# Kernel tuning notes

Hardware: AMD Instinct MI355X
Metric: run time of the kernel (lower is better)

Reference implementation:

```python
import jax, jax.numpy as jnp
import numpy as np

HEADS = 16
EPS = 1e-5

def _ln(x, g, b):
    m = jnp.mean(x, axis=-1, keepdims=True)
    v = jnp.mean((x - m) ** 2, axis=-1, keepdims=True)
    return (x - m) * jax.lax.rsqrt(v + EPS) * g + b

def setup_inputs() -> dict:
    key = jax.random.key(0)
    ks = jax.random.split(key, 12)
    B, N, C, H = 4, 2048, 1024, 4096
    d = {}
    d['x'] = jax.random.normal(ks[0], (B, N, C), jnp.float32)
    d['pos_embed'] = jax.random.normal(ks[1], (1, N, C), jnp.float32)
    # LayerNorm params (normq, normk, normv, norm)
    for nm in ['nq', 'nk', 'nv', 'n']:
        d[nm + '_g'] = jnp.ones((C,), jnp.float32)
        d[nm + '_b'] = jnp.zeros((C,), jnp.float32)
    s = 1.0 / np.sqrt(C)
    d['wq'] = jax.random.uniform(ks[2], (C, C), jnp.float32, -s, s)
    d['bq'] = jnp.zeros((C,), jnp.float32)
    d['wk'] = jax.random.uniform(ks[3], (C, C), jnp.float32, -s, s)
    d['bk'] = jnp.zeros((C,), jnp.float32)
    d['wv'] = jax.random.uniform(ks[4], (C, C), jnp.float32, -s, s)
    d['bv'] = jnp.zeros((C,), jnp.float32)
    d['wp'] = jax.random.uniform(ks[5], (C, C), jnp.float32, -s, s)
    d['bp'] = jnp.zeros((C,), jnp.float32)
    d['w1'] = jax.random.uniform(ks[6], (C, H), jnp.float32, -s, s)
    d['b1'] = jnp.zeros((H,), jnp.float32)
    sh = 1.0 / np.sqrt(H)
    d['w2'] = jax.random.uniform(ks[7], (H, C), jnp.float32, -sh, sh)
    d['b2'] = jnp.zeros((C,), jnp.float32)
    return d

def reference(x, pos_embed, nq_g, nq_b, nk_g, nk_b, nv_g, nv_b, wq, bq, wk, bk, wv, bv, wp, bp, n_g, n_b, w1, b1, w2, b2):
    B, N, C = x.shape
    hd = C // HEADS
    scale = hd ** -0.5
    q_in = x
    k_in = x + pos_embed
    v_in = x + pos_embed
    # Attention (eval mode: dropout = identity)
    q = (_ln(q_in, nq_g, nq_b) @ wq + bq).reshape(B, N, HEADS, hd)
    k = (_ln(k_in, nk_g, nk_b) @ wk + bk).reshape(B, N, HEADS, hd)
    v = (_ln(v_in, nv_g, nv_b) @ wv + bv).reshape(B, N, HEADS, hd)
    attn = jnp.einsum('bqhd,bkhd->bhqk', q, k) * scale
    attn = jax.nn.softmax(attn, axis=-1)
    out = jnp.einsum('bhqk,bkhd->bqhd', attn, v).reshape(B, N, C)
    out = out @ wp + bp
    # residual + MLP
    h = q_in + out
    y = _ln(h, n_g, n_b) @ w1 + b1
    y = jnp.where(y >= 0, y, 0.1 * y)  # LeakyReLU(0.1)
    y = y @ w2 + b2
    return h + y
```

## Files before the change

### kernel.cpp

```cpp
#include <hip/hip_runtime.h>
#include <hip/hip_bf16.h>

#define DEV __device__ __forceinline__

typedef __attribute__((ext_vector_type(8))) short short8;
typedef __attribute__((ext_vector_type(4))) short short4v;
typedef __attribute__((ext_vector_type(4))) float f32x4;
typedef __attribute__((ext_vector_type(2))) int int2v;

constexpr int Bb   = 4;
constexpr int SEQ  = 2048;
constexpr int C    = 1024;
constexpr int HID  = 4096;
constexpr int NH   = 16;
constexpr int HD   = 64;
constexpr int MTOT = Bb * SEQ;

DEV unsigned bfbits(float f) {
  unsigned x = __float_as_uint(f);
  return (x + 0x7fffu + ((x >> 16) & 1u)) >> 16;
}

DEV short f2bf(float f) { return (short)bfbits(f); }

DEV unsigned packrn(float a, float b) {
  unsigned ua = __float_as_uint(a) + 0x8000u;
  unsigned ub = __float_as_uint(b) + 0x8000u;
  return __builtin_amdgcn_perm(ub, ua, 0x07060302u);
}

DEV float fexp2(float x) {
#if __has_builtin(__builtin_amdgcn_exp2f)
  return __builtin_amdgcn_exp2f(x);
#else
  float r;
  asm("v_exp_f32 %0, %1" : "=v"(r) : "v"(x));
  return r;
#endif
}

DEV void gload16(const void* g, void* l) {
  __builtin_amdgcn_global_load_lds((const __attribute__((address_space(1))) void*)g,
                                   (__attribute__((address_space(3))) void*)l, 16, 0, 0);
}

DEV f32x4 mfma16(short4v a, short4v b, f32x4 c) {
#if __has_builtin(__builtin_amdgcn_mfma_f32_16x16x16bf16_1k)
  return __builtin_amdgcn_mfma_f32_16x16x16bf16_1k(a, b, c, 0, 0, 0);
#else
  asm volatile("v_mfma_f32_16x16x16_bf16 %0, %1, %2, %0" : "+v"(c) : "v"(a), "v"(b));
  return c;
#endif
}

DEV void transpose_body(const float* __restrict__ src, short* __restrict__ dst,
                        int R, int Cc) {
  __shared__ float t[32][33];
  int tx = threadIdx.x & 31, ty = threadIdx.x >> 5;
  int c0 = blockIdx.x * 32, r0 = blockIdx.y * 32;
  #pragma unroll
  for (int i = 0; i < 4; i++)
    t[ty + i * 8][tx] = src[(size_t)(r0 + ty + i * 8) * Cc + c0 + tx];
  __syncthreads();
  #pragma unroll
  for (int i = 0; i < 4; i++)
    dst[(size_t)(c0 + ty + i * 8) * R + r0 + tx] = f2bf(t[tx][ty + i * 8]);
}

__global__ void k_transpose_w(const float* __restrict__ src, short* __restrict__ dst,
                              int R, int Cc) {
  transpose_body(src, dst, R, Cc);
}

__global__ void k_transpose_w4(const float* __restrict__ s0, const float* __restrict__ s1,
                               const float* __restrict__ s2, const float* __restrict__ s3,
                               short* __restrict__ d0, short* __restrict__ d1,
                               short* __restrict__ d2, short* __restrict__ d3) {
  const float* s = blockIdx.z == 0 ? s0 : blockIdx.z == 1 ? s1 : blockIdx.z == 2 ? s2 : s3;
  short*       d = blockIdx.z == 0 ? d0 : blockIdx.z == 1 ? d1 : blockIdx.z == 2 ? d2 : d3;
  transpose_body(s, d, C, C);
}

__global__ void k_transpose_v(const short* __restrict__ V, short* __restrict__ Vt) {
  __shared__ short t[32][33];
  int tx = threadIdx.x & 31, ty = threadIdx.x >> 5;
  int plane = blockIdx.z;
  int b = plane >> 4, h = plane & 15;
  int n0 = blockIdx.x * 32, d0 = blockIdx.y * 32;
  #pragma unroll
  for (int i = 0; i < 4; i++)
    t[ty + i * 8][tx] = V[(size_t)(b * SEQ + n0 + ty + i * 8) * C + h * HD + d0 + tx];
  __syncthreads();
  #pragma unroll
  for (int i = 0; i < 4; i++)
    Vt[((size_t)plane * HD + d0 + ty + i * 8) * SEQ + n0 + tx] = t[tx][ty + i * 8];
}

__global__ void k_ln_qkv(const float* __restrict__ x, const float* __restrict__ pos,
                         const float* __restrict__ nqg, const float* __restrict__ nqb,
                         const float* __restrict__ nkg, const float* __restrict__ nkb,
                         const float* __restrict__ nvg, const float* __restrict__ nvb,
                         short* __restrict__ xq, short* __restrict__ xk,
                         short* __restrict__ xv) {
  int row = blockIdx.x, tid = threadIdx.x;
  int n = row & (SEQ - 1);
  float a4[4], p4[4];
  float s1 = 0, s2 = 0, t1 = 0, t2 = 0;
  #pragma unroll
  for (int i = 0; i < 4; i++) {
    int c = tid + i * 256;
    float a = x[(size_t)row * C + c];
    float p = pos[(size_t)n * C + c] + a;
    a4[i] = a; p4[i] = p;
    s1 += a; s2 += a * a; t1 += p; t2 += p * p;
  }
  #pragma unroll
  for (int off = 32; off; off >>= 1) {
    s1 += __shfl_xor(s1, off, 64);
    s2 += __shfl_xor(s2, off, 64);
    t1 += __shfl_xor(t1, off, 64);
    t2 += __shfl_xor(t2, off, 64);
  }
  __shared__ float red[4][4];
  int wave = tid >> 6, lane = tid & 63;
  if (lane == 0) { red[wave][0] = s1; red[wave][1] = s2; red[wave][2] = t1; red[wave][3] = t2; }
  __syncthreads();
  s1 = red[0][0] + red[1][0] + red[2][0] + red[3][0];
  s2 = red[0][1] + red[1][1] + red[2][1] + red[3][1];
  t1 = red[0][2] + red[1][2] + red[2][2] + red[3][2];
  t2 = red[0][3] + red[1][3] + red[2][3] + red[3][3];
  float mq = s1 * (1.f / C), mk = t1 * (1.f / C);
  float rq = rsqrtf(s2 * (1.f / C) - mq * mq + 1e-5f);
  float rk = rsqrtf(t2 * (1.f / C) - mk * mk + 1e-5f);
  #pragma unroll
  for (int i = 0; i < 4; i++) {
    int c = tid + i * 256;
    float nq_ = (a4[i] - mq) * rq;
    float nk_ = (p4[i] - mk) * rk;
    xq[(size_t)row * C + c] = f2bf(nq_ * nqg[c] + nqb[c]);
    xk[(size_t)row * C + c] = f2bf(nk_ * nkg[c] + nkb[c]);
    xv[(size_t)row * C + c] = f2bf(nk_ * nvg[c] + nvb[c]);
  }
}

__global__ void k_ln1(const float* __restrict__ h, const float* __restrict__ g,
                      const float* __restrict__ bta, short* __restrict__ out) {
  int row = blockIdx.x, tid = threadIdx.x;
  float a4[4];
  float s1 = 0, s2 = 0;
  #pragma unroll
  for (int i = 0; i < 4; i++) {
    int c = tid + i * 256;
    float a = h[(size_t)row * C + c];
    a4[i] = a; s1 += a; s2 += a * a;
  }
  #pragma unroll
  for (int off = 32; off; off >>= 1) {
    s1 += __shfl_xor(s1, off, 64);
    s2 += __shfl_xor(s2, off, 64);
  }
  __shared__ float red[4][2];
  int wave = tid >> 6, lane = tid & 63;
  if (lane == 0) { red[wave][0] = s1; red[wave][1] = s2; }
  __syncthreads();
  s1 = red[0][0] + red[1][0] + red[2][0] + red[3][0];
  s2 = red[0][1] + red[1][1] + red[2][1] + red[3][1];
  float m = s1 * (1.f / C);
  float r = rsqrtf(s2 * (1.f / C) - m * m + 1e-5f);
  #pragma unroll
  for (int i = 0; i < 4; i++) {
    int c = tid + i * 256;
    out[(size_t)row * C + c] = f2bf((a4[i] - m) * r * g[c] + bta[c]);
  }
}

template <typename EPI>
DEV void gemm_body(const short* __restrict__ A, const short* __restrict__ Bt,
                   int Kk, short* sA, short* sB, EPI&& epi) {
  const int tid = threadIdx.x;
  const int wave = tid >> 6, lane = tid & 63, quad = lane >> 4, l15 = lane & 15;
  const int wm = (wave >> 1) * 64, wn = (wave & 1) * 64;
  constexpr int BO = 128 * 32;

  const int r0 = tid >> 2, s0 = (tid & 3) * 8;
  const short* gA0 = A + (size_t)r0 * Kk + s0;
  const short* gA1 = A + (size_t)(r0 + 64) * Kk + s0;
  const short* gB0 = Bt + (size_t)r0 * Kk + s0;
  const short* gB1 = Bt + (size_t)(r0 + 64) * Kk + s0;
  short* lA0 = &sA[tid * 8];
  short* lA1 = &sA[(tid + 256) * 8];
  short* lB0 = &sB[tid * 8];
  short* lB1 = &sB[(tid + 256) * 8];

  const f32x4 fzero = {0.f, 0.f, 0.f, 0.f};
  f32x4 acc[4][4];
  #pragma unroll
  for (int mi = 0; mi < 4; mi++)
    #pragma unroll
    for (int ni = 0; ni < 4; ni++) acc[mi][ni] = fzero;

  gload16(gA0, lA0);
  gload16(gA1, lA1);
  gload16(gB0, lB0);
  gload16(gB1, lB1);

  for (int k0 = 0; k0 < Kk; k0 += 32) {
    const int buf = (k0 >> 5) & 1;
    __syncthreads();
    if (k0 + 32 < Kk) {
      const int bo = (buf ^ 1) * BO;
      gload16(gA0 + k0 + 32, lA0 + bo);
      gload16(gA1 + k0 + 32, lA1 + bo);
      gload16(gB0 + k0 + 32, lB0 + bo);
      gload16(gB1 + k0 + 32, lB1 + bo);
    }
    const int bo = buf * BO;
    short8 av[4], bv[4];
    #pragma unroll
    for (int mi = 0; mi < 4; mi++)
      av[mi] = *(const short8*)&sA[bo + (wm + mi * 16 + l15) * 32 + quad * 8];
    #pragma unroll
    for (int ni = 0; ni < 4; ni++)
      bv[ni] = *(const short8*)&sB[bo + (wn + ni * 16 + l15) * 32 + quad * 8];
    #pragma unroll
    for (int mi = 0; mi < 4; mi++)
      #pragma unroll
      for (int ni = 0; ni < 4; ni++)
        acc[mi][ni] = __builtin_amdgcn_mfma_f32_16x16x32_bf16(av[mi], bv[ni], acc[mi][ni], 0, 0, 0);
  }
  epi(acc, wm, wn, quad, l15);
}

template <int MODE>
__global__ __launch_bounds__(256, 2)
void k_gemm(const short* __restrict__ A, const short* __restrict__ Bt,
            const float* __restrict__ bias, const float* __restrict__ resid,
            void* __restrict__ outp, int Nn, int Kk) {
  __shared__ short sA[2 * 128 * 32];
  __shared__ short sB[2 * 128 * 32];
  const int m0 = blockIdx.x * 128, n0 = blockIdx.y * 128;
  gemm_body(A + (size_t)m0 * Kk, Bt + (size_t)n0 * Kk, Kk, sA, sB,
    [&](f32x4 (&acc)[4][4], int wm, int wn, int quad, int l15) {
      float bb[4];
      #pragma unroll
      for (int ni = 0; ni < 4; ni++) bb[ni] = bias[n0 + wn + ni * 16 + l15];
      #pragma unroll
      for (int mi = 0; mi < 4; mi++) {
        #pragma unroll
        for (int ni = 0; ni < 4; ni++) {
          #pragma unroll
          for (int r = 0; r < 4; r++) {
            int row = m0 + wm + mi * 16 + quad * 4 + r;
            int col = n0 + wn + ni * 16 + l15;
            float v = acc[mi][ni][r] + bb[ni];
            if constexpr (MODE == 1) v = v >= 0.f ? v : 0.1f * v;
            if constexpr (MODE == 2)
              ((float*)outp)[(size_t)row * Nn + col] = resid[(size_t)row * Nn + col] + v;
            else
              ((short*)outp)[(size_t)row * Nn + col] = f2bf(v);
          }
        }
      }
    });
}

template <int MODE>
__global__ __launch_bounds__(256, 2)
void k_gemm_p3(const short* __restrict__ A, const short* __restrict__ Bt,
               const float* __restrict__ bias, const float* __restrict__ resid,
               void* __restrict__ outp, int Nn, int Kk) {
  __shared__ short sA[3 * 128 * 32];
  __shared__ short sB[3 * 128 * 32];
  constexpr int BO = 128 * 32;
  const int tid = threadIdx.x;
  const int wave = tid >> 6, lane = tid & 63, quad = lane >> 4, l15 = lane & 15;
  const int wm = (wave >> 1) * 64, wn = (wave & 1) * 64;
  const int m0 = blockIdx.x * 128, n0 = blockIdx.y * 128;
  const short* Ab = A + (size_t)m0 * Kk;
  const short* Bb_ = Bt + (size_t)n0 * Kk;

  const int r0 = tid >> 2, s0 = (tid & 3) * 8;
  const short* gA0 = Ab + (size_t)r0 * Kk + s0;
  const short* gA1 = Ab + (size_t)(r0 + 64) * Kk + s0;
  const short* gB0 = Bb_ + (size_t)r0 * Kk + s0;
  const short* gB1 = Bb_ + (size_t)(r0 + 64) * Kk + s0;
  short* lA0 = &sA[tid * 8];
  short* lA1 = &sA[(tid + 256) * 8];
  short* lB0 = &sB[tid * 8];
  short* lB1 = &sB[(tid + 256) * 8];

  const f32x4 fzero = {0.f, 0.f, 0.f, 0.f};
  f32x4 acc[4][4];
  #pragma unroll
  for (int mi = 0; mi < 4; mi++)
    #pragma unroll
    for (int ni = 0; ni < 4; ni++) acc[mi][ni] = fzero;

  const int nk = Kk >> 5;

#define STG(j) {                                        \
    const int bo_ = ((j) % 3) * BO;                     \
    const int kk_ = (j) << 5;                           \
    gload16(gA0 + kk_, lA0 + bo_);                      \
    gload16(gA1 + kk_, lA1 + bo_);                      \
    gload16(gB0 + kk_, lB0 + bo_);                      \
    gload16(gB1 + kk_, lB1 + bo_); }

  STG(0)
  if (nk > 1) STG(1)

  for (int k = 0; k < nk; k++) {
    if (k + 1 < nk) asm volatile("s_waitcnt vmcnt(4)" ::: "memory");
    else            asm volatile("s_waitcnt vmcnt(0)" ::: "memory");
    __builtin_amdgcn_s_barrier();
    if (k + 2 < nk) STG(k + 2)
    const int bo = (k % 3) * BO;
    short8 av[4], bv[4];
    #pragma unroll
    for (int mi = 0; mi < 4; mi++)
      av[mi] = *(const short8*)&sA[bo + (wm + mi * 16 + l15) * 32 + quad * 8];
    #pragma unroll
    for (int ni = 0; ni < 4; ni++)
      bv[ni] = *(const short8*)&sB[bo + (wn + ni * 16 + l15) * 32 + quad * 8];
    #pragma unroll
    for (int mi = 0; mi < 4; mi++)
      #pragma unroll
      for (int ni = 0; ni < 4; ni++)
        acc[mi][ni] = __builtin_amdgcn_mfma_f32_16x16x32_bf16(av[mi], bv[ni], acc[mi][ni], 0, 0, 0);
  }
#undef STG

  float bb[4];
  #pragma unroll
  for (int ni = 0; ni < 4; ni++) bb[ni] = bias[n0 + wn + ni * 16 + l15];
  #pragma unroll
  for (int mi = 0; mi < 4; mi++) {
    #pragma unroll
    for (int ni = 0; ni < 4; ni++) {
      #pragma unroll
      for (int r = 0; r < 4; r++) {
        int row = m0 + wm + mi * 16 + quad * 4 + r;
        int col = n0 + wn + ni * 16 + l15;
        float v = acc[mi][ni][r] + bb[ni];
        if constexpr (MODE == 1) v = v >= 0.f ? v : 0.1f * v;
        if constexpr (MODE == 2)
          ((float*)outp)[(size_t)row * Nn + col] = resid[(size_t)row * Nn + col] + v;
        else
          ((short*)outp)[(size_t)row * Nn + col] = f2bf(v);
      }
    }
  }
}

__global__ __launch_bounds__(256, 2)
void k_gemm_qkv(const short* __restrict__ xq, const short* __restrict__ xk,
                const short* __restrict__ xv,
                const short* __restrict__ wqT, const short* __restrict__ wkT,
                const short* __restrict__ wvT,
                const float* __restrict__ bq, const float* __restrict__ bk,
                const float* __restrict__ bv,
                short* __restrict__ Qm, short* __restrict__ Km, short* __restrict__ Vm) {
  __shared__ short sA[2 * 128 * 32];
  __shared__ short sB[2 * 128 * 32];
  const int z = blockIdx.z;
  const short* A    = z == 0 ? xq : z == 1 ? xk : xv;
  const short* Bt   = z == 0 ? wqT : z == 1 ? wkT : wvT;
  const float* bias = z == 0 ? bq : z == 1 ? bk : bv;
  short* outp       = z == 0 ? Qm : z == 1 ? Km : Vm;
  const float scale = z == 0 ? 0.1803368801111244f : 1.0f;
  const int m0 = blockIdx.x * 128, n0 = blockIdx.y * 128;
  gemm_body(A + (size_t)m0 * C, Bt + (size_t)n0 * C, C, sA, sB,
    [&](f32x4 (&acc)[4][4], int wm, int wn, int quad, int l15) {
      float bb[4];
      #pragma unroll
      for (int ni = 0; ni < 4; ni++) bb[ni] = bias[n0 + wn + ni * 16 + l15];
      #pragma unroll
      for (int mi = 0; mi < 4; mi++)
        #pragma unroll
        for (int ni = 0; ni < 4; ni++)
          #pragma unroll
          for (int r = 0; r < 4; r++) {
            int row = m0 + wm + mi * 16 + quad * 4 + r;
            int col = n0 + wn + ni * 16 + l15;
            outp[(size_t)row * C + col] = f2bf((acc[mi][ni][r] + bb[ni]) * scale);
          }
    });
}

__global__ __launch_bounds__(256, 4)
void k_attn(const short* __restrict__ Q, const short* __restrict__ K,
            const short* __restrict__ Vt, short* __restrict__ O) {
  __shared__ __align__(16) short sK[2][64 * 64];
  __shared__ __align__(16) short sV[2][64 * 64];
  const int tid = threadIdx.x;
  const int bh = blockIdx.x;
  const int b = bh >> 4, h = bh & 15;
  const int q0 = blockIdx.y * 128;
  const int wave = tid >> 6, lane = tid & 63, quad = lane >> 4, l15 = lane & 15;
  const int wm = wave * 32;
  const size_t tokBase = (size_t)b * SEQ;

  short8 qf[2][2];
  #pragma unroll
  for (int qi = 0; qi < 2; qi++)
    #pragma unroll
    for (int hf = 0; hf < 2; hf++)
      qf[qi][hf] = *(const short8*)(Q + (tokBase + q0 + wm + qi * 16 + l15) * C
                                    + h * HD + hf * 32 + quad * 8);

  const int r0 = tid >> 3,        c0s = ((tid & 7) ^ (r0 & 7)) * 8;
  const int r1 = (tid + 256) >> 3, c1s = ((tid & 7) ^ (r1 & 7)) * 8;
  const short* gK0 = K + (tokBase + r0) * C + h * HD + c0s;
  const short* gK1 = K + (tokBase + r1) * C + h * HD + c1s;
  const short* gV0 = Vt + ((size_t)bh * HD + r0) * SEQ + c0s;
  const short* gV1 = Vt + ((size_t)bh * HD + r1) * SEQ + c1s;
  short* lK0 = &sK[0][tid * 8];
  short* lK1 = &sK[0][(tid + 256) * 8];
  short* lV0 = &sV[0][tid * 8];
  short* lV1 = &sV[0][(tid + 256) * 8];
  constexpr int BUFO = 64 * 64;

#define STAGE(bufsel, kb) {                                   \
    int kk = (kb) * 64, bo = (bufsel) * BUFO;                 \
    gload16(gK0 + (size_t)kk * C, lK0 + bo);                  \
    gload16(gK1 + (size_t)kk * C, lK1 + bo);                  \
    gload16(gV0 + kk,             lV0 + bo);                  \
    gload16(gV1 + kk,             lV1 + bo); }

  const f32x4 fzero = {0.f, 0.f, 0.f, 0.f};
  const short4v onesv = {0x3F80, 0x3F80, 0x3F80, 0x3F80};
  f32x4 o[2][4];
  f32x4 oSum[2] = {fzero, fzero};
  #pragma unroll
  for (int qi = 0; qi < 2; qi++)
    #pragma unroll
    for (int di = 0; di < 4; di++) o[qi][di] = fzero;

  const int sw = l15 & 7;

  STAGE(0, 0)

  for (int kb = 0; kb < SEQ / 64; kb++) {
    const int buf = kb & 1;
    __syncthreads();
    if (kb + 1 < SEQ / 64) STAGE(buf ^ 1, kb + 1)

    unsigned pk[4][2][2];
    #pragma unroll
    for (int ki = 0; ki < 4; ki++) {
      const int krow = (ki * 16 + l15) * 64;
      short8 a0 = *(const short8*)&sK[buf][krow + ((0 + quad) ^ sw) * 8];
      short8 a1 = *(const short8*)&sK[buf][krow + ((4 + quad) ^ sw) * 8];
      #pragma unroll
      for (int qi = 0; qi < 2; qi++) {
        f32x4 st = __builtin_amdgcn_mfma_f32_16x16x32_bf16(a0, qf[qi][0], fzero, 0, 0, 0);
        st = __builtin_amdgcn_mfma_f32_16x16x32_bf16(a1, qf[qi][1], st, 0, 0, 0);
        float p0 = fexp2(st[0]), p1 = fexp2(st[1]);
        float p2 = fexp2(st[2]), p3 = fexp2(st[3]);
        pk[ki][qi][0] = packrn(p0, p1);
        pk[ki][qi][1] = packrn(p2, p3);
      }
    }

    #pragma unroll
    for (int ki = 0; ki < 4; ki++) {
      short4v bv[4];
      const int g = ((ki * 2 + (quad >> 1)) ^ sw) * 8 + (quad & 1) * 4;
      #pragma unroll
      for (int di = 0; di < 4; di++)
        bv[di] = *(const short4v*)&sV[buf][(di * 16 + l15) * 64 + g];
      #pragma unroll
      for (int qi = 0; qi < 2; qi++) {
        int2v t; t.x = (int)pk[ki][qi][0]; t.y = (int)pk[ki][qi][1];
        short4v aP = __builtin_bit_cast(short4v, t);
        oSum[qi] = mfma16(aP, onesv, oSum[qi]);
        #pragma unroll
        for (int di = 0; di < 4; di++)
          o[qi][di] = mfma16(aP, bv[di], o[qi][di]);
      }
    }
  }
#undef STAGE

  float linv[2][4];
  #pragma unroll
  for (int qi = 0; qi < 2; qi++)
    #pragma unroll
    for (int r = 0; r < 4; r++)
      linv[qi][r] = 1.0f / oSum[qi][r];

  #pragma unroll
  for (int qi = 0; qi < 2; qi++)
    #pragma unroll
    for (int di = 0; di < 4; di++)
      #pragma unroll
      for (int r = 0; r < 4; r++) {
        int row = q0 + wm + qi * 16 + quad * 4 + r;
        int col = h * HD + di * 16 + l15;
        O[(tokBase + row) * C + col] = f2bf(o[qi][di][r] * linv[qi][r]);
      }
}

extern "C" void kernel_launch(void* const* d_in, const int* in_sizes, int n_in,
                              void* d_out, int out_size, void* d_ws, size_t ws_size,
                              hipStream_t stream) {
  const float* x   = (const float*)d_in[0];
  const float* pos = (const float*)d_in[1];
  const float* nqg = (const float*)d_in[2];
  const float* nqb = (const float*)d_in[3];
  const float* nkg = (const float*)d_in[4];
  const float* nkb = (const float*)d_in[5];
  const float* nvg = (const float*)d_in[6];
  const float* nvb = (const float*)d_in[7];
  const float* ng  = (const float*)d_in[8];
  const float* nb  = (const float*)d_in[9];
  const float* wq  = (const float*)d_in[10];
  const float* bq  = (const float*)d_in[11];
  const float* wk  = (const float*)d_in[12];
  const float* bk  = (const float*)d_in[13];
  const float* wv  = (const float*)d_in[14];
  const float* bv  = (const float*)d_in[15];
  const float* wp  = (const float*)d_in[16];
  const float* bp  = (const float*)d_in[17];
  const float* w1  = (const float*)d_in[18];
  const float* b1  = (const float*)d_in[19];
  const float* w2  = (const float*)d_in[20];
  const float* b2  = (const float*)d_in[21];

  char* ws = (char*)d_ws;
  const size_t MB = 1u << 20;
  short* wqT  = (short*)(ws + 0 * MB);
  short* wkT  = (short*)(ws + 2 * MB);
  short* wvT  = (short*)(ws + 4 * MB);
  short* wpT  = (short*)(ws + 6 * MB);
  short* w1T  = (short*)(ws + 8 * MB);
  short* w2T  = (short*)(ws + 16 * MB);
  short* xq   = (short*)(ws + 24 * MB);
  short* xk   = (short*)(ws + 40 * MB);
  short* xv   = (short*)(ws + 56 * MB);
  short* Qm   = (short*)(ws + 72 * MB);
  short* Km   = (short*)(ws + 88 * MB);
  short* Vm   = (short*)(ws + 104 * MB);
  short* Vt   = (short*)(ws + 120 * MB);
  short* y1   = (short*)(ws + 72 * MB);
  short* Ob   = xk;
  short* hln  = xq;
  float* hbuf = (float*)(ws + 136 * MB);
  (void)ws_size; (void)in_sizes; (void)n_in; (void)out_size;

  dim3 blk(256);
  k_transpose_w4<<<dim3(32, 32, 4), blk, 0, stream>>>(wq, wk, wv, wp, wqT, wkT, wvT, wpT);
  k_transpose_w<<<dim3(128, 32), blk, 0, stream>>>(w1, w1T, C, HID);
  k_transpose_w<<<dim3(32, 128), blk, 0, stream>>>(w2, w2T, HID, C);
  k_ln_qkv<<<dim3(MTOT), blk, 0, stream>>>(x, pos, nqg, nqb, nkg, nkb, nvg, nvb, xq, xk, xv);
  k_gemm_qkv<<<dim3(MTOT / 128, C / 128, 3), blk, 0, stream>>>(xq, xk, xv, wqT, wkT, wvT,
                                                               bq, bk, bv, Qm, Km, Vm);
  k_transpose_v<<<dim3(SEQ / 32, HD / 32, Bb * NH), blk, 0, stream>>>(Vm, Vt);
  k_attn<<<dim3(Bb * NH, SEQ / 128), blk, 0, stream>>>(Qm, Km, Vt, Ob);
  k_gemm<2><<<dim3(MTOT / 128, C / 128), blk, 0, stream>>>(Ob, wpT, bp, x, hbuf, C, C);
  k_ln1<<<dim3(MTOT), blk, 0, stream>>>(hbuf, ng, nb, hln);
  k_gemm<1><<<dim3(MTOT / 128, HID / 128), blk, 0, stream>>>(hln, w1T, b1, nullptr, y1, HID, C);
  k_gemm_p3<2><<<dim3(MTOT / 128, C / 128), blk, 0, stream>>>(y1, w2T, b2, hbuf, (float*)d_out, C, HID);
}
```

Measured before the change: 538.0 us.

## Replace down-projection GEMM with 8-wave 128x256 tile, swizzled LDS and phased MFMA

The final MLP down-projection GEMM (K=4096) moves to a new kernel with 512 threads, a 128x256 output tile, K-step 64, and double buffering. LDS rows are XOR-swizzled to avoid bank conflicts. The MFMA work is split into four barrier-separated phases with raised wave priority, and the block index is remapped for L2 locality. The goal is higher arithmetic intensity and better overlap of loads with MFMAs. In exchange, occupancy drops to one block per CU and the extra per-phase barriers may stall waves.

```diff
diff --git a/kernel.cpp b/kernel.cpp
--- a/kernel.cpp
+++ b/kernel.cpp
@@ -264,30 +264,78 @@
     });
 }
 
+template <int Q>
+DEV void phase8(const short* __restrict__ sAb, const short* __restrict__ sBb,
+                f32x4 (&acc)[4][4], int wm, int wn, int quad, int l15) {
+  constexpr int mis = (Q & 1) * 2, nis = (Q >> 1) * 2;
+  short8 av[2][2], bv[2][2];
+  #pragma unroll
+  for (int m2 = 0; m2 < 2; m2++) {
+    const int rA = wm + (mis + m2) * 16 + l15;
+    const int sw = rA & 7;
+    #pragma unroll
+    for (int ks = 0; ks < 2; ks++)
+      av[m2][ks] = *(const short8*)&sAb[rA * 64 + ((ks * 4 + quad) ^ sw) * 8];
+  }
+  #pragma unroll
+  for (int n2 = 0; n2 < 2; n2++) {
+    const int rB = wn + (nis + n2) * 16 + l15;
+    const int sw = rB & 7;
+    #pragma unroll
+    for (int ks = 0; ks < 2; ks++)
+      bv[n2][ks] = *(const short8*)&sBb[rB * 64 + ((ks * 4 + quad) ^ sw) * 8];
+  }
+  __builtin_amdgcn_s_barrier();
+  asm volatile("s_waitcnt lgkmcnt(0)" ::: "memory");
+  __builtin_amdgcn_sched_barrier(0);
+  __builtin_amdgcn_s_setprio(1);
+  #pragma unroll
+  for (int ks = 0; ks < 2; ks++)
+    #pragma unroll
+    for (int m2 = 0; m2 < 2; m2++)
+      #pragma unroll
+      for (int n2 = 0; n2 < 2; n2++)
+        acc[mis + m2][nis + n2] = __builtin_amdgcn_mfma_f32_16x16x32_bf16(
+            av[m2][ks], bv[n2][ks], acc[mis + m2][nis + n2], 0, 0, 0);
+  __builtin_amdgcn_s_setprio(0);
+  __builtin_amdgcn_s_barrier();
+}
+
 template <int MODE>
-__global__ __launch_bounds__(256, 2)
-void k_gemm_p3(const short* __restrict__ A, const short* __restrict__ Bt,
-               const float* __restrict__ bias, const float* __restrict__ resid,
-               void* __restrict__ outp, int Nn, int Kk) {
-  __shared__ short sA[3 * 128 * 32];
-  __shared__ short sB[3 * 128 * 32];
-  constexpr int BO = 128 * 32;
+__global__ __launch_bounds__(512, 1)
+void k_gemm8(const short* __restrict__ A, const short* __restrict__ Bt,
+             const float* __restrict__ bias, const float* __restrict__ resid,
+             void* __restrict__ outp, int Nn, int Kk) {
+  __shared__ __align__(16) short sA[2][128 * 64];
+  __shared__ __align__(16) short sB[2][256 * 64];
   const int tid = threadIdx.x;
   const int wave = tid >> 6, lane = tid & 63, quad = lane >> 4, l15 = lane & 15;
-  const int wm = (wave >> 1) * 64, wn = (wave & 1) * 64;
-  const int m0 = blockIdx.x * 128, n0 = blockIdx.y * 128;
-  const short* Ab = A + (size_t)m0 * Kk;
-  const short* Bb_ = Bt + (size_t)n0 * Kk;
-
-  const int r0 = tid >> 2, s0 = (tid & 3) * 8;
-  const short* gA0 = Ab + (size_t)r0 * Kk + s0;
-  const short* gA1 = Ab + (size_t)(r0 + 64) * Kk + s0;
-  const short* gB0 = Bb_ + (size_t)r0 * Kk + s0;
-  const short* gB1 = Bb_ + (size_t)(r0 + 64) * Kk + s0;
-  short* lA0 = &sA[tid * 8];
-  short* lA1 = &sA[(tid + 256) * 8];
-  short* lB0 = &sB[tid * 8];
-  short* lB1 = &sB[(tid + 256) * 8];
+  const int wm = (wave >> 2) * 64, wn = (wave & 3) * 64;
+
+  const int gx = gridDim.x;
+  const int nwg = gx * gridDim.y;
+  const int orig = blockIdx.y * gx + blockIdx.x;
+  const int swz = (orig & 7) * (nwg >> 3) + (orig >> 3);
+  const int m0 = (swz % gx) * 128, n0 = (swz / gx) * 256;
+
+  const int sr = tid >> 3, su = tid & 7;
+  const int sx = (su ^ (sr & 7)) * 8;
+  const short* gA0 = A + (size_t)(m0 + sr) * Kk + sx;
+  const short* gA1 = gA0 + (size_t)64 * Kk;
+  const short* gB0 = Bt + (size_t)(n0 + sr) * Kk + sx;
+  const short* gB1 = gB0 + (size_t)64 * Kk;
+  const short* gB2 = gB0 + (size_t)128 * Kk;
+  const short* gB3 = gB0 + (size_t)192 * Kk;
+
+  auto stg = [&](int t) {
+    const int b_ = t & 1, ko = t << 6;
+    gload16(gA0 + ko, &sA[b_][(size_t)tid * 8]);
+    gload16(gA1 + ko, &sA[b_][(size_t)(512 + tid) * 8]);
+    gload16(gB0 + ko, &sB[b_][(size_t)tid * 8]);
+    gload16(gB1 + ko, &sB[b_][(size_t)(512 + tid) * 8]);
+    gload16(gB2 + ko, &sB[b_][(size_t)(1024 + tid) * 8]);
+    gload16(gB3 + ko, &sB[b_][(size_t)(1536 + tid) * 8]);
+  };
 
   const f32x4 fzero = {0.f, 0.f, 0.f, 0.f};
   f32x4 acc[4][4];
@@ -296,39 +344,31 @@
     #pragma unroll
     for (int ni = 0; ni < 4; ni++) acc[mi][ni] = fzero;
 
-  const int nk = Kk >> 5;
-
-#define STG(j) {                                        \
-    const int bo_ = ((j) % 3) * BO;                     \
-    const int kk_ = (j) << 5;                           \
-    gload16(gA0 + kk_, lA0 + bo_);                      \
-    gload16(gA1 + kk_, lA1 + bo_);                      \
-    gload16(gB0 + kk_, lB0 + bo_);                      \
-    gload16(gB1 + kk_, lB1 + bo_); }
-
-  STG(0)
-  if (nk > 1) STG(1)
-
-  for (int k = 0; k < nk; k++) {
-    if (k + 1 < nk) asm volatile("s_waitcnt vmcnt(4)" ::: "memory");
-    else            asm volatile("s_waitcnt vmcnt(0)" ::: "memory");
+  const int nkt = Kk >> 6;
+  stg(0);
+  for (int t = 0; t < nkt; t += 2) {
+    if (t + 1 < nkt) { stg(t + 1); asm volatile("s_waitcnt vmcnt(6)" ::: "memory"); }
+    else             {             asm volatile("s_waitcnt vmcnt(0)" ::: "memory"); }
     __builtin_amdgcn_s_barrier();
-    if (k + 2 < nk) STG(k + 2)
-    const int bo = (k % 3) * BO;
-    short8 av[4], bv[4];
-    #pragma unroll
-    for (int mi = 0; mi < 4; mi++)
-      av[mi] = *(const short8*)&sA[bo + (wm + mi * 16 + l15) * 32 + quad * 8];
-    #pragma unroll
-    for (int ni = 0; ni < 4; ni++)
-      bv[ni] = *(const short8*)&sB[bo + (wn + ni * 16 + l15) * 32 + quad * 8];
-    #pragma unroll
-    for (int mi = 0; mi < 4; mi++)
-      #pragma unroll
-      for (int ni = 0; ni < 4; ni++)
-        acc[mi][ni] = __builtin_amdgcn_mfma_f32_16x16x32_bf16(av[mi], bv[ni], acc[mi][ni], 0, 0, 0);
-  }
-#undef STG
+    {
+      const short* a_ = &sA[t & 1][0]; const short* b_ = &sB[t & 1][0];
+      phase8<0>(a_, b_, acc, wm, wn, quad, l15);
+      phase8<1>(a_, b_, acc, wm, wn, quad, l15);
+      phase8<2>(a_, b_, acc, wm, wn, quad, l15);
+      phase8<3>(a_, b_, acc, wm, wn, quad, l15);
+    }
+    if (t + 1 >= nkt) break;
+    if (t + 2 < nkt) { stg(t + 2); asm volatile("s_waitcnt vmcnt(6)" ::: "memory"); }
+    else             {             asm volatile("s_waitcnt vmcnt(0)" ::: "memory"); }
+    __builtin_amdgcn_s_barrier();
+    {
+      const short* a_ = &sA[(t + 1) & 1][0]; const short* b_ = &sB[(t + 1) & 1][0];
+      phase8<0>(a_, b_, acc, wm, wn, quad, l15);
+      phase8<1>(a_, b_, acc, wm, wn, quad, l15);
+      phase8<2>(a_, b_, acc, wm, wn, quad, l15);
+      phase8<3>(a_, b_, acc, wm, wn, quad, l15);
+    }
+  }
 
   float bb[4];
   #pragma unroll
@@ -560,5 +600,6 @@
   k_gemm<2><<<dim3(MTOT / 128, C / 128), blk, 0, stream>>>(Ob, wpT, bp, x, hbuf, C, C);
   k_ln1<<<dim3(MTOT), blk, 0, stream>>>(hbuf, ng, nb, hln);
   k_gemm<1><<<dim3(MTOT / 128, HID / 128), blk, 0, stream>>>(hln, w1T, b1, nullptr, y1, HID, C);
-  k_gemm_p3<2><<<dim3(MTOT / 128, C / 128), blk, 0, stream>>>(y1, w2T, b2, hbuf, (float*)d_out, C, HID);
-}
+  k_gemm8<2><<<dim3(MTOT / 128, C / 256), dim3(512), 0, stream>>>(y1, w2T, b2, hbuf,
+                                                                  (float*)d_out, C, HID);
+}
```

Result: slower. 566.2 us (+5.2%).
